# Optimization experiments

Measured on AMD Instinct MI355X. Metric: run time of the kernel, lower is better.

The kernel has to match this reference:

```python
import jax, jax.numpy as jnp
import numpy as np

G, N, E = 8, 10000, 160000
D_IN, D_H, D_OUT = 300, 256, 128
EPS = 1e-5


def setup_inputs() -> dict:
    key = jax.random.key(0)
    ks = jax.random.split(key, 4)
    x = jax.random.normal(ks[0], (G, N, D_IN), dtype=jnp.float32)
    edge_index = jax.random.randint(ks[1], (G, 2, E), 0, N)
    W1 = jax.random.normal(ks[2], (D_IN, D_H), dtype=jnp.float32) * (1.0 / np.sqrt(D_IN))
    b1 = jnp.zeros((D_H,), jnp.float32)
    g1 = jnp.ones((D_H,), jnp.float32)
    be1 = jnp.zeros((D_H,), jnp.float32)
    W2 = jax.random.normal(ks[3], (D_H, D_OUT), dtype=jnp.float32) * (1.0 / np.sqrt(D_H))
    b2 = jnp.zeros((D_OUT,), jnp.float32)
    g2 = jnp.ones((D_OUT,), jnp.float32)
    be2 = jnp.zeros((D_OUT,), jnp.float32)
    return dict(x=x, edge_index=edge_index, W1=W1, b1=b1, g1=g1, be1=be1,
                W2=W2, b2=b2, g2=g2, be2=be2)


def _gcn_conv(x, src, dst, W, b):
    # PyG GCNConv: h = xW; add self-loops; sym-normalized aggregation; + bias
    h = x @ W                                   # [N, F_out]
    deg = jnp.ones((N,), h.dtype).at[dst].add(1.0)  # in-degree + self-loop
    dinv = jax.lax.rsqrt(deg)                   # deg >= 1 always
    coef = dinv[src] * dinv[dst]                # [E]
    agg = jax.ops.segment_sum(h[src] * coef[:, None], dst, num_segments=N)
    agg = agg + h * (dinv * dinv)[:, None]      # self-loop term
    return agg + b


def _layernorm(x, g, b):
    mu = jnp.mean(x, axis=-1, keepdims=True)
    var = jnp.mean(jnp.square(x - mu), axis=-1, keepdims=True)
    return (x - mu) * jax.lax.rsqrt(var + EPS) * g + b


def _forward_one(xg, eg, W1, b1, g1, be1, W2, b2, g2, be2):
    src, dst = eg[0], eg[1]
    h = jax.nn.relu(_gcn_conv(xg, src, dst, W1, b1))
    h = _layernorm(h, g1, be1)
    h = _gcn_conv(h, src, dst, W2, b2)
    return _layernorm(h, g2, be2)


def reference(x, edge_index, W1, b1, g1, be1, W2, b2, g2, be2):
    f = jax.vmap(lambda xg, eg: _forward_one(xg, eg, W1, b1, g1, be1, W2, b2, g2, be2))
    return f(x, edge_index)  # [G, N, D_OUT]
```

## Files before the change

### kernel.cpp

```cpp
#include <hip/hip_runtime.h>
#include <hip/hip_bf16.h>

#define GG   8
#define NN   10000
#define EE   160000
#define DIN  300
#define KP1  320
#define DH   256
#define DOUT 128
#define MTOT 80000
#define LN_EPS 1e-5f

typedef short bf16x8 __attribute__((ext_vector_type(8)));
typedef float f32x4  __attribute__((ext_vector_type(4)));
typedef ushort u16x8 __attribute__((ext_vector_type(8)));

__device__ inline float bf2f(ushort u) {
    union { unsigned int i; float f; } x;
    x.i = ((unsigned int)u) << 16;
    return x.f;
}
__device__ inline ushort f2b(float f) {
    union { float f; unsigned int u; } x;
    x.f = f;
    unsigned int u = x.u;
    return (ushort)((u + 0x7fffu + ((u >> 16) & 1u)) >> 16);
}
__device__ inline short bcvt(float f) {
    __hip_bfloat16 h = __float2bfloat16(f);
    return *reinterpret_cast<short*>(&h);
}

__global__ __launch_bounds__(256) void k_util(const float* __restrict__ W1,
                                              const float* __restrict__ W2,
                                              ushort* __restrict__ w1t,
                                              ushort* __restrict__ w2t,
                                              int* __restrict__ cnt) {
    int i = blockIdx.x * blockDim.x + threadIdx.x;
    if (i < GG * NN) cnt[i] = 0;
    if (i < DH * KP1) {
        int n = i / KP1, k = i % KP1;
        w1t[i] = (k < DIN) ? f2b(W1[(size_t)k * DH + n]) : 0;
    }
    if (i < DOUT * DH) {
        int n = i / DH, k = i % DH;
        w2t[i] = f2b(W2[(size_t)k * DOUT + n]);
    }
}

__global__ __launch_bounds__(256) void k_count(const int* __restrict__ ei,
                                               int* __restrict__ cnt,
                                               int* __restrict__ slot) {
    int bid = blockIdx.x;
    int g = bid & 7;
    int e = (bid >> 3) * 256 + threadIdx.x;
    int dst = ei[(size_t)g * 2 * EE + EE + e];
    slot[(size_t)g * EE + e] = atomicAdd(&cnt[g * NN + dst], 1);
}

__global__ void k_scan(const int* __restrict__ cnt, int* __restrict__ rowptr,
                       float* __restrict__ dinv) {
    int g = blockIdx.x;
    int t = threadIdx.x;
    const int per = (NN + 255) / 256;
    __shared__ int sums[256];
    __shared__ int offs[257];
    int base = t * per;
    int s = 0;
    for (int i = 0; i < per; i++) {
        int n = base + i;
        if (n < NN) s += cnt[g * NN + n];
    }
    sums[t] = s;
    __syncthreads();
    if (t == 0) {
        int acc = 0;
        for (int i = 0; i < 256; i++) { offs[i] = acc; acc += sums[i]; }
        offs[256] = acc;
    }
    __syncthreads();
    int run = offs[t];
    for (int i = 0; i < per; i++) {
        int n = base + i;
        if (n < NN) {
            int c = cnt[g * NN + n];
            rowptr[g * (NN + 1) + n] = run;
            dinv[g * NN + n] = 1.0f / sqrtf(1.0f + (float)c);
            run += c;
        }
    }
    if (t == 255) rowptr[g * (NN + 1) + NN] = offs[256];
}

__global__ __launch_bounds__(256) void k_fill(const int* __restrict__ ei,
                                              const int* __restrict__ rowptr,
                                              const int* __restrict__ slot,
                                              const float* __restrict__ dinv,
                                              int2* __restrict__ edges) {
    int bid = blockIdx.x;
    int g = bid & 7;
    int e = (bid >> 3) * 256 + threadIdx.x;
    int src = ei[(size_t)g * 2 * EE + e];
    int dst = ei[(size_t)g * 2 * EE + EE + e];
    int pos = rowptr[g * (NN + 1) + dst] + slot[(size_t)g * EE + e];
    float coef = dinv[g * NN + src] * dinv[g * NN + dst];
    int2 rec;
    rec.x = src;
    rec.y = __float_as_int(coef);
    edges[(size_t)g * EE + pos] = rec;
}

__global__ __launch_bounds__(512) void k_gemm1(const float* __restrict__ x,
                                               const ushort* __restrict__ Bt,
                                               ushort* __restrict__ C) {
    __shared__ ushort Bs[64 * 328];
    const int tid = threadIdx.x;
    const int lane = tid & 63;
    const int w = tid >> 6;
    const int n0 = blockIdx.x * 64;
    const int fr = lane & 15;
    const int fk = (lane >> 4) * 8;

    for (int idx = tid; idx < 64 * 40; idx += 512) {
        const int r = idx / 40, c8 = (idx - r * 40) * 8;
        *(u16x8*)&Bs[r * 328 + c8] = *(const u16x8*)&Bt[(size_t)(n0 + r) * KP1 + c8];
    }
    __syncthreads();

    const int rbase = blockIdx.y * 256 + w * 32;
    const float* xr0 = x + (size_t)min(rbase + fr,      MTOT - 1) * DIN;
    const float* xr1 = x + (size_t)min(rbase + 16 + fr, MTOT - 1) * DIN;

    f32x4 acc[2][4];
#pragma unroll
    for (int g = 0; g < 2; g++)
#pragma unroll
        for (int j = 0; j < 4; j++) acc[g][j] = (f32x4){0.f, 0.f, 0.f, 0.f};

#pragma unroll
    for (int kk = 0; kk < 10; kk++) {
        const int kb = kk * 32 + fk;
        const int c0 = min(kb, DIN - 4);
        const int c1 = min(kb + 4, DIN - 4);
        f32x4 p0 = *(const f32x4*)(xr0 + c0);
        f32x4 q0 = *(const f32x4*)(xr0 + c1);
        f32x4 p1 = *(const f32x4*)(xr1 + c0);
        f32x4 q1 = *(const f32x4*)(xr1 + c1);
        bf16x8 a0, a1;
        a0[0] = bcvt(p0[0]); a0[1] = bcvt(p0[1]); a0[2] = bcvt(p0[2]); a0[3] = bcvt(p0[3]);
        a0[4] = bcvt(q0[0]); a0[5] = bcvt(q0[1]); a0[6] = bcvt(q0[2]); a0[7] = bcvt(q0[3]);
        a1[0] = bcvt(p1[0]); a1[1] = bcvt(p1[1]); a1[2] = bcvt(p1[2]); a1[3] = bcvt(p1[3]);
        a1[4] = bcvt(q1[0]); a1[5] = bcvt(q1[1]); a1[6] = bcvt(q1[2]); a1[7] = bcvt(q1[3]);
        bf16x8 bv[4];
#pragma unroll
        for (int j = 0; j < 4; j++)
            bv[j] = *(const bf16x8*)&Bs[(j * 16 + fr) * 328 + kb];
#pragma unroll
        for (int j = 0; j < 4; j++) {
            acc[0][j] = __builtin_amdgcn_mfma_f32_16x16x32_bf16(a0, bv[j], acc[0][j], 0, 0, 0);
            acc[1][j] = __builtin_amdgcn_mfma_f32_16x16x32_bf16(a1, bv[j], acc[1][j], 0, 0, 0);
        }
    }

#pragma unroll
    for (int g = 0; g < 2; g++) {
        const int row0 = rbase + g * 16 + (lane >> 4) * 4;
#pragma unroll
        for (int j = 0; j < 4; j++) {
            const int col = n0 + j * 16 + fr;
#pragma unroll
            for (int q = 0; q < 4; q++) {
                const int row = row0 + q;
                if (row < MTOT)
                    C[(size_t)row * DH + col] = f2b(acc[g][j][q]);
            }
        }
    }
}

__global__ __launch_bounds__(512) void k_gemm2(const ushort* __restrict__ A,
                                               const ushort* __restrict__ Bt,
                                               ushort* __restrict__ C) {
    __shared__ ushort Bs[128 * 264];
    const int tid = threadIdx.x;
    const int lane = tid & 63;
    const int w = tid >> 6;
    const int fr = lane & 15;
    const int fk = (lane >> 4) * 8;

    for (int idx = tid; idx < 128 * 32; idx += 512) {
        const int r = idx >> 5, c8 = (idx & 31) * 8;
        *(u16x8*)&Bs[r * 264 + c8] = *(const u16x8*)&Bt[(size_t)r * DH + c8];
    }
    __syncthreads();

    const int rbase = blockIdx.x * 256 + w * 32;
    const ushort* ar0 = A + (size_t)min(rbase + fr,      MTOT - 1) * DH;
    const ushort* ar1 = A + (size_t)min(rbase + 16 + fr, MTOT - 1) * DH;

    f32x4 acc[2][8];
#pragma unroll
    for (int g = 0; g < 2; g++)
#pragma unroll
        for (int j = 0; j < 8; j++) acc[g][j] = (f32x4){0.f, 0.f, 0.f, 0.f};

#pragma unroll
    for (int kk = 0; kk < 8; kk++) {
        const int kb = kk * 32 + fk;
        bf16x8 a0 = *(const bf16x8*)(ar0 + kb);
        bf16x8 a1 = *(const bf16x8*)(ar1 + kb);
#pragma unroll
        for (int j = 0; j < 8; j++) {
            bf16x8 bv = *(const bf16x8*)&Bs[(j * 16 + fr) * 264 + kb];
            acc[0][j] = __builtin_amdgcn_mfma_f32_16x16x32_bf16(a0, bv, acc[0][j], 0, 0, 0);
            acc[1][j] = __builtin_amdgcn_mfma_f32_16x16x32_bf16(a1, bv, acc[1][j], 0, 0, 0);
        }
    }

#pragma unroll
    for (int g = 0; g < 2; g++) {
        const int row0 = rbase + g * 16 + (lane >> 4) * 4;
#pragma unroll
        for (int j = 0; j < 8; j++) {
            const int col = j * 16 + fr;
#pragma unroll
            for (int q = 0; q < 4; q++) {
                const int row = row0 + q;
                if (row < MTOT)
                    C[(size_t)row * DOUT + col] = f2b(acc[g][j][q]);
            }
        }
    }
}

template <int D, bool RELU, typename OutT>
__global__ __launch_bounds__(256) void k_agg(const ushort* __restrict__ h,
                                             const int* __restrict__ rowptr,
                                             const int2* __restrict__ edges,
                                             const float* __restrict__ dinv,
                                             const float* __restrict__ bias,
                                             const float* __restrict__ gam,
                                             const float* __restrict__ bet,
                                             OutT* __restrict__ out) {
    constexpr int F = 8;
    constexpr int GL = D / F;
    constexpr int NPW = 64 / GL;
    __shared__ int2 s_rec[4][64];
    const int tid = threadIdx.x;
    const int lane = tid & 63;
    const int wv = tid >> 6;
    const int grp = lane / GL;
    const int gl = lane & (GL - 1);
    const int fb = gl * F;
    const int g = blockIdx.x & 7;
    const int n = (blockIdx.x >> 3) * (4 * NPW) + wv * NPW + grp;
    const ushort* hg = h + (size_t)g * NN * D;
    const int2* eg = edges + (size_t)g * EE;
    const int r0 = rowptr[g * (NN + 1) + n];
    const int r1 = rowptr[g * (NN + 1) + n + 1];
    const float dn = dinv[g * NN + n];
    int2* srw = &s_rec[wv][grp * GL];

    float acc[F];
#pragma unroll
    for (int i = 0; i < F; i++) acc[i] = 0.f;

    for (int base = r0; base < r1; base += GL) {
        const int c = min(GL, r1 - base);
        int2 rec;
        rec.x = 0;
        rec.y = 0;
        if (gl < c) rec = eg[base + gl];
        srw[gl] = rec;
        const int cpad = (c + 3) & ~3;
        for (int j = 0; j < cpad; j += 4) {
            const int4 ra = *(const int4*)&srw[j];
            const int4 rb = *(const int4*)&srw[j + 2];
            u16x8 v0 = *(const u16x8*)&hg[(size_t)ra.x * D + fb];
            u16x8 v1 = *(const u16x8*)&hg[(size_t)ra.z * D + fb];
            u16x8 v2 = *(const u16x8*)&hg[(size_t)rb.x * D + fb];
            u16x8 v3 = *(const u16x8*)&hg[(size_t)rb.z * D + fb];
            const float w0 = __int_as_float(ra.y);
            const float w1 = __int_as_float(ra.w);
            const float w2 = __int_as_float(rb.y);
            const float w3 = __int_as_float(rb.w);
#pragma unroll
            for (int i = 0; i < F; i++) acc[i] = fmaf(bf2f(v0[i]), w0, acc[i]);
#pragma unroll
            for (int i = 0; i < F; i++) acc[i] = fmaf(bf2f(v1[i]), w1, acc[i]);
#pragma unroll
            for (int i = 0; i < F; i++) acc[i] = fmaf(bf2f(v2[i]), w2, acc[i]);
#pragma unroll
            for (int i = 0; i < F; i++) acc[i] = fmaf(bf2f(v3[i]), w3, acc[i]);
        }
    }

    {
        const float ws = dn * dn;
        u16x8 v = *(const u16x8*)&hg[(size_t)n * D + fb];
#pragma unroll
        for (int i = 0; i < F; i++) {
            acc[i] = fmaf(bf2f(v[i]), ws, acc[i]);
            acc[i] += bias[fb + i];
            if (RELU) acc[i] = fmaxf(acc[i], 0.f);
        }
    }
    float s1 = 0.f, s2 = 0.f;
#pragma unroll
    for (int i = 0; i < F; i++) { s1 += acc[i]; s2 += acc[i] * acc[i]; }
#pragma unroll
    for (int o = GL / 2; o > 0; o >>= 1) {
        s1 += __shfl_xor(s1, o);
        s2 += __shfl_xor(s2, o);
    }
    const float mu = s1 / D;
    const float rs = rsqrtf(s2 / D - mu * mu + LN_EPS);

    if constexpr (sizeof(OutT) == 2) {
        u16x8 o;
#pragma unroll
        for (int i = 0; i < F; i++)
            o[i] = f2b((acc[i] - mu) * rs * gam[fb + i] + bet[fb + i]);
        *(u16x8*)&((ushort*)out)[((size_t)g * NN + n) * D + fb] = o;
    } else {
        float* op = &((float*)out)[((size_t)g * NN + n) * D + fb];
        float4 oa, ob;
        oa.x = (acc[0] - mu) * rs * gam[fb + 0] + bet[fb + 0];
        oa.y = (acc[1] - mu) * rs * gam[fb + 1] + bet[fb + 1];
        oa.z = (acc[2] - mu) * rs * gam[fb + 2] + bet[fb + 2];
        oa.w = (acc[3] - mu) * rs * gam[fb + 3] + bet[fb + 3];
        ob.x = (acc[4] - mu) * rs * gam[fb + 4] + bet[fb + 4];
        ob.y = (acc[5] - mu) * rs * gam[fb + 5] + bet[fb + 5];
        ob.z = (acc[6] - mu) * rs * gam[fb + 6] + bet[fb + 6];
        ob.w = (acc[7] - mu) * rs * gam[fb + 7] + bet[fb + 7];
        *(float4*)&op[0] = oa;
        *(float4*)&op[4] = ob;
    }
}

extern "C" void kernel_launch(void* const* d_in, const int* in_sizes, int n_in,
                              void* d_out, int out_size, void* d_ws, size_t ws_size,
                              hipStream_t stream) {
    const float* x   = (const float*)d_in[0];
    const int*   ei  = (const int*)d_in[1];
    const float* W1  = (const float*)d_in[2];
    const float* b1  = (const float*)d_in[3];
    const float* g1  = (const float*)d_in[4];
    const float* be1 = (const float*)d_in[5];
    const float* W2  = (const float*)d_in[6];
    const float* b2  = (const float*)d_in[7];
    const float* g2  = (const float*)d_in[8];
    const float* be2 = (const float*)d_in[9];
    float* out = (float*)d_out;

    char* w = (char*)d_ws;
    ushort* w1t  = (ushort*)w;                        w += (size_t)DH * KP1 * 2;
    ushort* w2t  = (ushort*)w;                        w += (size_t)DOUT * DH * 2;
    ushort* h1b  = (ushort*)w;                        w += (size_t)MTOT * DH * 2;
    ushort* out1 = (ushort*)w;                        w += (size_t)MTOT * DH * 2;
    int*   cnt    = (int*)w;                          w += (size_t)GG * NN * 4;
    int*   rowptr = (int*)w;                          w += (size_t)GG * (NN + 1) * 4 + 224;
    int*   slot   = (int*)w;                          w += (size_t)GG * EE * 4;
    float* dinv   = (float*)w;                        w += (size_t)GG * NN * 4;
    int2*  edges  = (int2*)w;
    ushort* h2b = h1b;

    k_util<<<dim3((DH * KP1 + 255) / 256), dim3(256), 0, stream>>>(W1, W2, w1t, w2t, cnt);

    k_count<<<dim3((EE / 256) * GG), dim3(256), 0, stream>>>(ei, cnt, slot);
    k_scan<<<dim3(GG), dim3(256), 0, stream>>>(cnt, rowptr, dinv);
    k_fill<<<dim3((EE / 256) * GG), dim3(256), 0, stream>>>(ei, rowptr, slot, dinv, edges);

    k_gemm1<<<dim3(4, (MTOT + 255) / 256), dim3(512), 0, stream>>>(x, w1t, h1b);

    k_agg<DH, true, ushort><<<dim3((NN / 8) * GG), dim3(256), 0, stream>>>(
        h1b, rowptr, edges, dinv, b1, g1, be1, out1);

    k_gemm2<<<dim3((MTOT + 255) / 256), dim3(512), 0, stream>>>(out1, w2t, h2b);

    k_agg<DOUT, false, float><<<dim3((NN / 16) * GG), dim3(256), 0, stream>>>(
        h2b, rowptr, edges, dinv, b2, g2, be2, out);
}
```

Before: 267.0 us.

## Restructure GEMMs to keep A rows in registers and swizzle LDS B tiles

gemm1 now has each block own 128 rows across all 256 output columns. The fp32 x rows are read and converted to bf16 once into registers, instead of being re-read by four column blocks. B is staged in 64-column quarters with LDS double buffering, and the LDS layout uses an XOR swizzle in place of padding to avoid bank conflicts. gemm2 likewise holds A fragments in registers with 16 rows per wave and a swizzled B tile. Register pressure rises (10 bf16x8 A fragments plus 16 accumulators), and the row-bound checks are dropped because MTOT divides evenly by 128.

```diff
diff --git a/kernel.cpp b/kernel.cpp
--- a/kernel.cpp
+++ b/kernel.cpp
@@ -113,123 +113,126 @@
 __global__ __launch_bounds__(512) void k_gemm1(const float* __restrict__ x,
                                                const ushort* __restrict__ Bt,
                                                ushort* __restrict__ C) {
-    __shared__ ushort Bs[64 * 328];
-    const int tid = threadIdx.x;
-    const int lane = tid & 63;
-    const int w = tid >> 6;
-    const int n0 = blockIdx.x * 64;
-    const int fr = lane & 15;
-    const int fk = (lane >> 4) * 8;
-
-    for (int idx = tid; idx < 64 * 40; idx += 512) {
-        const int r = idx / 40, c8 = (idx - r * 40) * 8;
-        *(u16x8*)&Bs[r * 328 + c8] = *(const u16x8*)&Bt[(size_t)(n0 + r) * KP1 + c8];
-    }
-    __syncthreads();
-
-    const int rbase = blockIdx.y * 256 + w * 32;
-    const float* xr0 = x + (size_t)min(rbase + fr,      MTOT - 1) * DIN;
-    const float* xr1 = x + (size_t)min(rbase + 16 + fr, MTOT - 1) * DIN;
-
-    f32x4 acc[2][4];
-#pragma unroll
-    for (int g = 0; g < 2; g++)
-#pragma unroll
-        for (int j = 0; j < 4; j++) acc[g][j] = (f32x4){0.f, 0.f, 0.f, 0.f};
-
-#pragma unroll
-    for (int kk = 0; kk < 10; kk++) {
-        const int kb = kk * 32 + fk;
-        const int c0 = min(kb, DIN - 4);
-        const int c1 = min(kb + 4, DIN - 4);
-        f32x4 p0 = *(const f32x4*)(xr0 + c0);
-        f32x4 q0 = *(const f32x4*)(xr0 + c1);
-        f32x4 p1 = *(const f32x4*)(xr1 + c0);
-        f32x4 q1 = *(const f32x4*)(xr1 + c1);
-        bf16x8 a0, a1;
-        a0[0] = bcvt(p0[0]); a0[1] = bcvt(p0[1]); a0[2] = bcvt(p0[2]); a0[3] = bcvt(p0[3]);
-        a0[4] = bcvt(q0[0]); a0[5] = bcvt(q0[1]); a0[6] = bcvt(q0[2]); a0[7] = bcvt(q0[3]);
-        a1[0] = bcvt(p1[0]); a1[1] = bcvt(p1[1]); a1[2] = bcvt(p1[2]); a1[3] = bcvt(p1[3]);
-        a1[4] = bcvt(q1[0]); a1[5] = bcvt(q1[1]); a1[6] = bcvt(q1[2]); a1[7] = bcvt(q1[3]);
-        bf16x8 bv[4];
-#pragma unroll
-        for (int j = 0; j < 4; j++)
-            bv[j] = *(const bf16x8*)&Bs[(j * 16 + fr) * 328 + kb];
-#pragma unroll
-        for (int j = 0; j < 4; j++) {
-            acc[0][j] = __builtin_amdgcn_mfma_f32_16x16x32_bf16(a0, bv[j], acc[0][j], 0, 0, 0);
-            acc[1][j] = __builtin_amdgcn_mfma_f32_16x16x32_bf16(a1, bv[j], acc[1][j], 0, 0, 0);
-        }
-    }
-
-#pragma unroll
-    for (int g = 0; g < 2; g++) {
-        const int row0 = rbase + g * 16 + (lane >> 4) * 4;
-#pragma unroll
-        for (int j = 0; j < 4; j++) {
-            const int col = n0 + j * 16 + fr;
-#pragma unroll
-            for (int q = 0; q < 4; q++) {
-                const int row = row0 + q;
-                if (row < MTOT)
-                    C[(size_t)row * DH + col] = f2b(acc[g][j][q]);
-            }
-        }
-    }
-}
-
-__global__ __launch_bounds__(512) void k_gemm2(const ushort* __restrict__ A,
-                                               const ushort* __restrict__ Bt,
-                                               ushort* __restrict__ C) {
-    __shared__ ushort Bs[128 * 264];
+    __shared__ ushort Bs[2][64 * 320];
     const int tid = threadIdx.x;
     const int lane = tid & 63;
     const int w = tid >> 6;
     const int fr = lane & 15;
-    const int fk = (lane >> 4) * 8;
+    const int hi = lane >> 4;
+    const int row = blockIdx.x * 128 + w * 16 + fr;
+    const float* xr = x + (size_t)row * DIN;
+
+    bf16x8 a[10];
+#pragma unroll
+    for (int kk = 0; kk < 10; kk++) {
+        const int kb = kk * 32 + hi * 8;
+        f32x4 p = *(const f32x4*)(xr + min(kb, DIN - 4));
+        f32x4 q = *(const f32x4*)(xr + min(kb + 4, DIN - 4));
+        a[kk][0] = bcvt(p[0]); a[kk][1] = bcvt(p[1]);
+        a[kk][2] = bcvt(p[2]); a[kk][3] = bcvt(p[3]);
+        a[kk][4] = bcvt(q[0]); a[kk][5] = bcvt(q[1]);
+        a[kk][6] = bcvt(q[2]); a[kk][7] = bcvt(q[3]);
+    }
+
+    auto stageQ = [&](int q, int buf) {
+        for (int idx = tid; idx < 64 * 40; idx += 512) {
+            const int r = idx / 40;
+            const int c = idx - r * 40;
+            const int cs = (c & ~7) | ((c & 7) ^ (r & 7));
+            *(u16x8*)&Bs[buf][r * 320 + cs * 8] =
+                *(const u16x8*)&Bt[(size_t)(q * 64 + r) * KP1 + c * 8];
+        }
+    };
+
+    f32x4 acc[4][4];
+#pragma unroll
+    for (int q = 0; q < 4; q++)
+#pragma unroll
+        for (int j = 0; j < 4; j++) acc[q][j] = (f32x4){0.f, 0.f, 0.f, 0.f};
+
+    stageQ(0, 0);
+    __syncthreads();
+#pragma unroll
+    for (int q = 0; q < 4; q++) {
+        const int buf = q & 1;
+        if (q < 3) stageQ(q + 1, buf ^ 1);
+#pragma unroll
+        for (int kk = 0; kk < 10; kk++) {
+            const int cb = kk * 4 + hi;
+#pragma unroll
+            for (int j = 0; j < 4; j++) {
+                const int r = j * 16 + fr;
+                const int cs = (cb & ~7) | ((cb & 7) ^ (r & 7));
+                bf16x8 bv = *(const bf16x8*)&Bs[buf][r * 320 + cs * 8];
+                acc[q][j] = __builtin_amdgcn_mfma_f32_16x16x32_bf16(a[kk], bv,
+                                                                    acc[q][j], 0, 0, 0);
+            }
+        }
+        if (q < 3) __syncthreads();
+    }
+
+    const int row0 = blockIdx.x * 128 + w * 16 + hi * 4;
+#pragma unroll
+    for (int q = 0; q < 4; q++)
+#pragma unroll
+        for (int j = 0; j < 4; j++) {
+            const int col = q * 64 + j * 16 + fr;
+#pragma unroll
+            for (int qq = 0; qq < 4; qq++)
+                C[(size_t)(row0 + qq) * DH + col] = f2b(acc[q][j][qq]);
+        }
+}
+
+__global__ __launch_bounds__(512) void k_gemm2(const ushort* __restrict__ A,
+                                               const ushort* __restrict__ Bt,
+                                               ushort* __restrict__ C) {
+    __shared__ ushort Bs[128 * 256];
+    const int tid = threadIdx.x;
+    const int lane = tid & 63;
+    const int w = tid >> 6;
+    const int fr = lane & 15;
+    const int hi = lane >> 4;
+    const int row = blockIdx.x * 128 + w * 16 + fr;
+    const ushort* ar = A + (size_t)row * DH;
+
+    bf16x8 a[8];
+#pragma unroll
+    for (int kk = 0; kk < 8; kk++)
+        a[kk] = *(const bf16x8*)(ar + kk * 32 + hi * 8);
 
     for (int idx = tid; idx < 128 * 32; idx += 512) {
-        const int r = idx >> 5, c8 = (idx & 31) * 8;
-        *(u16x8*)&Bs[r * 264 + c8] = *(const u16x8*)&Bt[(size_t)r * DH + c8];
+        const int r = idx >> 5;
+        const int c = idx & 31;
+        const int cs = (c & ~7) | ((c & 7) ^ (r & 7));
+        *(u16x8*)&Bs[r * 256 + cs * 8] =
+            *(const u16x8*)&Bt[(size_t)r * DH + c * 8];
     }
     __syncthreads();
 
-    const int rbase = blockIdx.x * 256 + w * 32;
-    const ushort* ar0 = A + (size_t)min(rbase + fr,      MTOT - 1) * DH;
-    const ushort* ar1 = A + (size_t)min(rbase + 16 + fr, MTOT - 1) * DH;
-
-    f32x4 acc[2][8];
-#pragma unroll
-    for (int g = 0; g < 2; g++)
-#pragma unroll
-        for (int j = 0; j < 8; j++) acc[g][j] = (f32x4){0.f, 0.f, 0.f, 0.f};
+    f32x4 acc[8];
+#pragma unroll
+    for (int j = 0; j < 8; j++) acc[j] = (f32x4){0.f, 0.f, 0.f, 0.f};
 
 #pragma unroll
     for (int kk = 0; kk < 8; kk++) {
-        const int kb = kk * 32 + fk;
-        bf16x8 a0 = *(const bf16x8*)(ar0 + kb);
-        bf16x8 a1 = *(const bf16x8*)(ar1 + kb);
+        const int cb = kk * 4 + hi;
 #pragma unroll
         for (int j = 0; j < 8; j++) {
-            bf16x8 bv = *(const bf16x8*)&Bs[(j * 16 + fr) * 264 + kb];
-            acc[0][j] = __builtin_amdgcn_mfma_f32_16x16x32_bf16(a0, bv, acc[0][j], 0, 0, 0);
-            acc[1][j] = __builtin_amdgcn_mfma_f32_16x16x32_bf16(a1, bv, acc[1][j], 0, 0, 0);
-        }
-    }
-
-#pragma unroll
-    for (int g = 0; g < 2; g++) {
-        const int row0 = rbase + g * 16 + (lane >> 4) * 4;
-#pragma unroll
-        for (int j = 0; j < 8; j++) {
-            const int col = j * 16 + fr;
-#pragma unroll
-            for (int q = 0; q < 4; q++) {
-                const int row = row0 + q;
-                if (row < MTOT)
-                    C[(size_t)row * DOUT + col] = f2b(acc[g][j][q]);
-            }
-        }
+            const int r = j * 16 + fr;
+            const int cs = (cb & ~7) | ((cb & 7) ^ (r & 7));
+            bf16x8 bv = *(const bf16x8*)&Bs[r * 256 + cs * 8];
+            acc[j] = __builtin_amdgcn_mfma_f32_16x16x32_bf16(a[kk], bv,
+                                                             acc[j], 0, 0, 0);
+        }
+    }
+
+    const int row0 = blockIdx.x * 128 + w * 16 + hi * 4;
+#pragma unroll
+    for (int j = 0; j < 8; j++) {
+        const int col = j * 16 + fr;
+#pragma unroll
+        for (int qq = 0; qq < 4; qq++)
+            C[(size_t)(row0 + qq) * DOUT + col] = f2b(acc[j][qq]);
     }
 }
 
@@ -371,12 +374,12 @@
     k_scan<<<dim3(GG), dim3(256), 0, stream>>>(cnt, rowptr, dinv);
     k_fill<<<dim3((EE / 256) * GG), dim3(256), 0, stream>>>(ei, rowptr, slot, dinv, edges);
 
-    k_gemm1<<<dim3(4, (MTOT + 255) / 256), dim3(512), 0, stream>>>(x, w1t, h1b);
+    k_gemm1<<<dim3(MTOT / 128), dim3(512), 0, stream>>>(x, w1t, h1b);
 
     k_agg<DH, true, ushort><<<dim3((NN / 8) * GG), dim3(256), 0, stream>>>(
         h1b, rowptr, edges, dinv, b1, g1, be1, out1);
 
-    k_gemm2<<<dim3((MTOT + 255) / 256), dim3(512), 0, stream>>>(out1, w2t, h2b);
+    k_gemm2<<<dim3(MTOT / 128), dim3(512), 0, stream>>>(out1, w2t, h2b);
 
     k_agg<DOUT, false, float><<<dim3((NN / 16) * GG), dim3(256), 0, stream>>>(
         h2b, rowptr, edges, dinv, b2, g2, be2, out);
```

Measured after the change: 235.1 us. 12.0% less time.
